# Kernel optimization log

Measured on AMD Instinct MI355X. Metric: run time of the kernel, lower is better.

The kernel has to match this reference:

```python
import jax, jax.numpy as jnp
import numpy as np

N, FIN, H, O, K = 300000, 128, 64, 32, 5


def setup_inputs() -> dict:
    key = jax.random.key(0)
    ks = jax.random.split(key, 8)
    xav_uh = (2.0 / (FIN + H)) ** 0.5  # xavier_normal scale for Linear(FIN, H)
    xav_ho = (2.0 / (H + O)) ** 0.5
    return {
        "user": jax.random.normal(ks[0], (N, FIN), dtype=jnp.float32),
        "item": jax.random.normal(ks[1], (N, FIN), dtype=jnp.float32),
        "r": jax.random.randint(ks[2], (N,), 0, K),
        "c": jax.random.uniform(ks[3], (N,), dtype=jnp.float32),
        # relation-stacked Linear weights, torch layout [out, in] -> [K, H, FIN]
        "Wu": jax.random.normal(ks[4], (K, H, FIN), dtype=jnp.float32) * xav_uh,
        "bu": jnp.zeros((K, H), dtype=jnp.float32),
        "Wv": jax.random.normal(ks[5], (K, H, FIN), dtype=jnp.float32) * xav_uh,
        "bv": jnp.zeros((K, H), dtype=jnp.float32),
        "Wl": jax.random.normal(ks[6], (O, H), dtype=jnp.float32) * xav_ho,
        "bl": jnp.zeros((O,), dtype=jnp.float32),
    }


def reference(user, item, r, c, Wu, bu, Wv, bv, Wl, bl):
    # Per-row relation-indexed linear: out[i] = x[i] @ W[r[i]].T + b[r[i]]
    def rel_linear(x, W, b):
        allp = jnp.einsum("ni,khi->nkh", x, W) + b[None]  # [N, K, H]
        return jnp.take_along_axis(allp, r[:, None, None], axis=1)[:, 0, :]  # [N, H]

    u_next = c[:, None] * rel_linear(item, Wu, bu)  # messages from items to users
    v_next = c[:, None] * rel_linear(user, Wv, bv)  # messages from users to items
    u_out = jax.nn.relu(jax.nn.relu(u_next) @ Wl.T + bl)
    v_out = jax.nn.relu(jax.nn.relu(v_next) @ Wl.T + bl)
    return (u_out, v_out)
```

## Files before the change

### kernel.cpp

```cpp
#include <hip/hip_runtime.h>
#include <hip/hip_bf16.h>

#define N_ROWS 300000
#define FIN    128
#define HDIM   64
#define ODIM   32
#define KREL   5
#define BRT    128
#define NTT    ((N_ROWS + BRT - 1) / BRT)
#define TPB    4
#define NCHUNK ((NTT + TPB - 1) / TPB)

typedef __attribute__((ext_vector_type(8))) short bf8_t;
typedef __attribute__((ext_vector_type(4))) float f32x4;
typedef __attribute__((ext_vector_type(4))) unsigned int u32x4;

static __device__ __forceinline__ unsigned pk2(float lo, float hi) {
  __hip_bfloat162 h = __float22bfloat162_rn(make_float2(lo, hi));
  return *reinterpret_cast<unsigned*>(&h);
}

static __device__ __forceinline__ bf8_t cvt8(float4 a, float4 b) {
  u32x4 u;
  u.x = pk2(a.x, a.y);
  u.y = pk2(a.z, a.w);
  u.z = pk2(b.x, b.y);
  u.w = pk2(b.z, b.w);
  return __builtin_bit_cast(bf8_t, u);
}

static __device__ __forceinline__ void stbf4_pk(void* base, int byte, float4 v) {
  unsigned long long p = (unsigned long long)pk2(v.x, v.y)
                       | ((unsigned long long)pk2(v.z, v.w) << 32);
  *(unsigned long long*)((char*)base + byte) = p;
}

static __device__ __forceinline__ bf8_t lds_load16(const void* base, int byte) {
  return *(const bf8_t*)((const char*)base + byte);
}


__global__ __launch_bounds__(512, 1) void gcn_main(
    const float* __restrict__ user, const float* __restrict__ item,
    const int* __restrict__ r, const float* __restrict__ c,
    const float* __restrict__ Wu, const float* __restrict__ bu,
    const float* __restrict__ Wv, const float* __restrict__ bv,
    const float* __restrict__ Wl, const float* __restrict__ bl,
    float* __restrict__ out)
{
  __shared__ __align__(16) unsigned short sW[KREL * HDIM * FIN];
  __shared__ __align__(16) unsigned short sX[BRT * FIN];
  __shared__ float sB[KREL * HDIM];

  const int tid   = threadIdx.x;
  const int side  = blockIdx.x & 1;
  const int chunk = blockIdx.x >> 1;
  const int t_begin = chunk * TPB;
  if (t_begin >= NTT) return;
  const int t_end = (t_begin + TPB < NTT) ? t_begin + TPB : NTT;

  const float* X  = side ? user : item;
  const float* Wk = side ? Wv : Wu;
  const float* bk = side ? bv : bu;

  const int lane = tid & 63;
  const int wid  = tid >> 6;
  const int lrow = lane & 15;
  const int lkg  = lane >> 4;
  const int sh   = lane >> 5;
  const int c4   = lane & 31;

  {
    const float4* w4 = (const float4*)Wk;
    #pragma unroll
    for (int j = 0; j < 20; ++j) {
      int f4   = j * 512 + tid;
      int k    = f4 >> 11;
      int rowk = (f4 >> 5) & 63;
      int cc   = f4 & 31;
      int byte = (k << 14) + ((rowk * 256 + cc * 8) ^ ((rowk & 7) << 4));
      stbf4_pk(sW, byte, w4[f4]);
    }
  }
  if (tid < KREL * HDIM) sB[tid] = bk[tid];

  bf8_t wl[2][2];
  #pragma unroll
  for (int n2 = 0; n2 < 2; ++n2)
    #pragma unroll
    for (int k2 = 0; k2 < 2; ++k2) {
      const float* p = Wl + (size_t)(n2 * 16 + lrow) * HDIM + k2 * 32 + lkg * 8;
      wl[n2][k2] = cvt8(*(const float4*)p, *(const float4*)(p + 4));
    }
  const float blv0 = bl[lrow];
  const float blv1 = bl[16 + lrow];

  char* myX = (char*)sX + wid * 4096;
  const int rowb_off = wid * 16;

  #pragma unroll
  for (int it = 0; it < 8; ++it) {
    int grow = t_begin * BRT + rowb_off + it * 2 + sh;
    grow = (grow < N_ROWS) ? grow : N_ROWS - 1;
    float4 a = *(const float4*)(X + (size_t)grow * FIN + c4 * 4);
    int rl   = it * 2 + sh;
    int byte = (rl * 256 + c4 * 8) ^ ((rl & 7) << 4);
    stbf4_pk(myX, byte, a);
  }
  __syncthreads();

  for (int t = t_begin; t < t_end; ++t) {
    const int tile0 = t * BRT;
    const bool do_stage = (t + 1 < t_end);

    int rowA = tile0 + rowb_off + lrow;
    int myrel = r[(rowA < N_ROWS) ? rowA : N_ROWS - 1];

    float4 ld[8];
    if (do_stage) {
      #pragma unroll
      for (int it = 0; it < 8; ++it) {
        int grow = tile0 + BRT + rowb_off + it * 2 + sh;
        grow = (grow < N_ROWS) ? grow : N_ROWS - 1;
        ld[it] = *(const float4*)(X + (size_t)grow * FIN + c4 * 4);
      }
    }

    const int erow = tile0 + rowb_off + lkg * 4;
    int rQ[4]; float cQ[4];
    #pragma unroll
    for (int q = 0; q < 4; ++q) {
      int rc = erow + q;
      rc = (rc < N_ROWS) ? rc : N_ROWS - 1;
      rQ[q] = r[rc];
      cQ[q] = c[rc];
    }

    __builtin_amdgcn_sched_barrier(0);

    f32x4 acc[4];
    #pragma unroll
    for (int n = 0; n < 4; ++n) acc[n] = f32x4{0.f, 0.f, 0.f, 0.f};

    const bf8_t zero8 = {};
    const int axor = (lrow & 7) << 4;
    #pragma unroll
    for (int kc = 0; kc < 4; ++kc) {
      const int kb = (kc * 32 + lkg * 8) * 2;
      bf8_t au = lds_load16(myX, (lrow * 256 + kb) ^ axor);
      #pragma unroll
      for (int k = 0; k < KREL; ++k) {
        bf8_t auk = (myrel == k) ? au : zero8;
        const int kofs = k << 14;
        #pragma unroll
        for (int n = 0; n < 4; ++n) {
          int brow = n * 16 + lrow;
          int bx   = kofs + ((brow * 256 + kb) ^ ((brow & 7) << 4));
          acc[n] = __builtin_amdgcn_mfma_f32_16x16x32_bf16(auk, lds_load16(sW, bx), acc[n], 0, 0, 0);
        }
      }
    }

    #pragma unroll
    for (int n = 0; n < 4; ++n) {
      int hcol = n * 16 + lrow;
      #pragma unroll
      for (int q = 0; q < 4; ++q) {
        int rr   = lkg * 4 + q;
        int byte = (rr * 128 + hcol * 2) ^ ((rr & 7) << 4);
        float bb = sB[rQ[q] * HDIM + hcol];
        float hv = fmaxf(cQ[q] * (acc[n][q] + bb), 0.f);
        *(unsigned short*)(myX + byte) = (unsigned short)(pk2(hv, hv) & 0xFFFFu);
      }
    }

    f32x4 acc2[2];
    acc2[0] = f32x4{0.f, 0.f, 0.f, 0.f};
    acc2[1] = f32x4{0.f, 0.f, 0.f, 0.f};
    #pragma unroll
    for (int k2 = 0; k2 < 2; ++k2) {
      const int kb = (k2 * 32 + lkg * 8) * 2;
      const int ax = (lrow * 128 + kb) ^ axor;
      bf8_t a2 = lds_load16(myX, ax);
      #pragma unroll
      for (int n2 = 0; n2 < 2; ++n2)
        acc2[n2] = __builtin_amdgcn_mfma_f32_16x16x32_bf16(a2, wl[n2][k2], acc2[n2], 0, 0, 0);
    }

    const size_t obase = (size_t)side * N_ROWS * ODIM;
    #pragma unroll
    for (int n2 = 0; n2 < 2; ++n2) {
      int col  = n2 * 16 + lrow;
      float bb = (n2 == 0) ? blv0 : blv1;
      #pragma unroll
      for (int q = 0; q < 4; ++q) {
        int row = erow + q;
        if (row < N_ROWS)
          out[obase + (size_t)row * ODIM + col] = fmaxf(acc2[n2][q] + bb, 0.f);
      }
    }

    __builtin_amdgcn_sched_barrier(0);

    if (do_stage) {
      #pragma unroll
      for (int it = 0; it < 8; ++it) {
        int rl   = it * 2 + sh;
        int byte = (rl * 256 + c4 * 8) ^ ((rl & 7) << 4);
        stbf4_pk(myX, byte, ld[it]);
      }
    }
  }
}

extern "C" void kernel_launch(void* const* d_in, const int* in_sizes, int n_in,
                              void* d_out, int out_size, void* d_ws, size_t ws_size,
                              hipStream_t stream) {
  const float* user = (const float*)d_in[0];
  const float* item = (const float*)d_in[1];
  const int*   r    = (const int*)d_in[2];
  const float* c    = (const float*)d_in[3];
  const float* Wu   = (const float*)d_in[4];
  const float* bu   = (const float*)d_in[5];
  const float* Wv   = (const float*)d_in[6];
  const float* bv   = (const float*)d_in[7];
  const float* Wl   = (const float*)d_in[8];
  const float* bl   = (const float*)d_in[9];
  float* out = (float*)d_out;

  gcn_main<<<2 * NCHUNK, 512, 0, stream>>>(user, item, r, c, Wu, bu, Wv, bv,
                                           Wl, bl, out);
}
```

Before: 113.3 us.

## Process two 16-row M-tiles per wave to reuse LDS weight fragments

Each wave now handles 32 rows instead of 16: the block tile grows to 256 rows and tiles per block drop to 2. Every weight fragment read from LDS feeds two MFMAs, halving weight LDS traffic per row, and the prefetch depth per thread doubles to 16 float4s. The cost is higher register pressure (twice the accumulators and staged loads) and an sX buffer that doubles to 64KB, bringing total LDS to about 146KB.

New measurement: 134.6 us. 18.8% more time.

```diff
diff --git a/kernel.cpp b/kernel.cpp
--- a/kernel.cpp
+++ b/kernel.cpp
@@ -6,9 +6,9 @@
 #define HDIM   64
 #define ODIM   32
 #define KREL   5
-#define BRT    128
+#define BRT    256
 #define NTT    ((N_ROWS + BRT - 1) / BRT)
-#define TPB    4
+#define TPB    2
 #define NCHUNK ((NTT + TPB - 1) / TPB)
 
 typedef __attribute__((ext_vector_type(8))) short bf8_t;
@@ -95,11 +95,11 @@
   const float blv0 = bl[lrow];
   const float blv1 = bl[16 + lrow];
 
-  char* myX = (char*)sX + wid * 4096;
-  const int rowb_off = wid * 16;
+  char* myX = (char*)sX + wid * 8192;
+  const int rowb_off = wid * 32;
 
   #pragma unroll
-  for (int it = 0; it < 8; ++it) {
+  for (int it = 0; it < 16; ++it) {
     int grow = t_begin * BRT + rowb_off + it * 2 + sh;
     grow = (grow < N_ROWS) ? grow : N_ROWS - 1;
     float4 a = *(const float4*)(X + (size_t)grow * FIN + c4 * 4);
@@ -112,51 +112,63 @@
   for (int t = t_begin; t < t_end; ++t) {
     const int tile0 = t * BRT;
     const bool do_stage = (t + 1 < t_end);
-
-    int rowA = tile0 + rowb_off + lrow;
-    int myrel = r[(rowA < N_ROWS) ? rowA : N_ROWS - 1];
-
-    float4 ld[8];
+    const int base = tile0 + rowb_off;
+
+    int ra0 = base + lrow;        ra0 = (ra0 < N_ROWS) ? ra0 : N_ROWS - 1;
+    int ra1 = base + 16 + lrow;   ra1 = (ra1 < N_ROWS) ? ra1 : N_ROWS - 1;
+    const int myrel0 = r[ra0];
+    const int myrel1 = r[ra1];
+
+    float4 ld[16];
     if (do_stage) {
       #pragma unroll
-      for (int it = 0; it < 8; ++it) {
-        int grow = tile0 + BRT + rowb_off + it * 2 + sh;
+      for (int it = 0; it < 16; ++it) {
+        int grow = base + BRT + it * 2 + sh;
         grow = (grow < N_ROWS) ? grow : N_ROWS - 1;
         ld[it] = *(const float4*)(X + (size_t)grow * FIN + c4 * 4);
       }
     }
 
-    const int erow = tile0 + rowb_off + lkg * 4;
-    int rQ[4]; float cQ[4];
-    #pragma unroll
-    for (int q = 0; q < 4; ++q) {
-      int rc = erow + q;
-      rc = (rc < N_ROWS) ? rc : N_ROWS - 1;
-      rQ[q] = r[rc];
-      cQ[q] = c[rc];
+    int rQ[2][4]; float cQ[2][4];
+    #pragma unroll
+    for (int h = 0; h < 2; ++h) {
+      #pragma unroll
+      for (int q = 0; q < 4; ++q) {
+        int rc = base + h * 16 + lkg * 4 + q;
+        rc = (rc < N_ROWS) ? rc : N_ROWS - 1;
+        rQ[h][q] = r[rc];
+        cQ[h][q] = c[rc];
+      }
     }
 
     __builtin_amdgcn_sched_barrier(0);
 
-    f32x4 acc[4];
-    #pragma unroll
-    for (int n = 0; n < 4; ++n) acc[n] = f32x4{0.f, 0.f, 0.f, 0.f};
+    f32x4 acc0[4], acc1[4];
+    #pragma unroll
+    for (int n = 0; n < 4; ++n) {
+      acc0[n] = f32x4{0.f, 0.f, 0.f, 0.f};
+      acc1[n] = f32x4{0.f, 0.f, 0.f, 0.f};
+    }
 
     const bf8_t zero8 = {};
     const int axor = (lrow & 7) << 4;
     #pragma unroll
     for (int kc = 0; kc < 4; ++kc) {
       const int kb = (kc * 32 + lkg * 8) * 2;
-      bf8_t au = lds_load16(myX, (lrow * 256 + kb) ^ axor);
+      bf8_t au0 = lds_load16(myX, ((lrow)      * 256 + kb) ^ axor);
+      bf8_t au1 = lds_load16(myX, ((16 + lrow) * 256 + kb) ^ axor);
       #pragma unroll
       for (int k = 0; k < KREL; ++k) {
-        bf8_t auk = (myrel == k) ? au : zero8;
+        bf8_t a0 = (myrel0 == k) ? au0 : zero8;
+        bf8_t a1 = (myrel1 == k) ? au1 : zero8;
         const int kofs = k << 14;
         #pragma unroll
         for (int n = 0; n < 4; ++n) {
           int brow = n * 16 + lrow;
           int bx   = kofs + ((brow * 256 + kb) ^ ((brow & 7) << 4));
-          acc[n] = __builtin_amdgcn_mfma_f32_16x16x32_bf16(auk, lds_load16(sW, bx), acc[n], 0, 0, 0);
+          bf8_t w = lds_load16(sW, bx);
+          acc0[n] = __builtin_amdgcn_mfma_f32_16x16x32_bf16(a0, w, acc0[n], 0, 0, 0);
+          acc1[n] = __builtin_amdgcn_mfma_f32_16x16x32_bf16(a1, w, acc1[n], 0, 0, 0);
         }
       }
     }
@@ -166,25 +178,39 @@
       int hcol = n * 16 + lrow;
       #pragma unroll
       for (int q = 0; q < 4; ++q) {
-        int rr   = lkg * 4 + q;
-        int byte = (rr * 128 + hcol * 2) ^ ((rr & 7) << 4);
-        float bb = sB[rQ[q] * HDIM + hcol];
-        float hv = fmaxf(cQ[q] * (acc[n][q] + bb), 0.f);
-        *(unsigned short*)(myX + byte) = (unsigned short)(pk2(hv, hv) & 0xFFFFu);
-      }
-    }
-
-    f32x4 acc2[2];
-    acc2[0] = f32x4{0.f, 0.f, 0.f, 0.f};
-    acc2[1] = f32x4{0.f, 0.f, 0.f, 0.f};
+        {
+          int rr   = lkg * 4 + q;
+          int byte = (rr * 128 + hcol * 2) ^ ((rr & 7) << 4);
+          float bb = sB[rQ[0][q] * HDIM + hcol];
+          float hv = fmaxf(cQ[0][q] * (acc0[n][q] + bb), 0.f);
+          *(unsigned short*)(myX + byte) = (unsigned short)(pk2(hv, hv) & 0xFFFFu);
+        }
+        {
+          int rr   = 16 + lkg * 4 + q;
+          int byte = (rr * 128 + hcol * 2) ^ ((rr & 7) << 4);
+          float bb = sB[rQ[1][q] * HDIM + hcol];
+          float hv = fmaxf(cQ[1][q] * (acc1[n][q] + bb), 0.f);
+          *(unsigned short*)(myX + byte) = (unsigned short)(pk2(hv, hv) & 0xFFFFu);
+        }
+      }
+    }
+
+    f32x4 acc2_0[2], acc2_1[2];
+    #pragma unroll
+    for (int n2 = 0; n2 < 2; ++n2) {
+      acc2_0[n2] = f32x4{0.f, 0.f, 0.f, 0.f};
+      acc2_1[n2] = f32x4{0.f, 0.f, 0.f, 0.f};
+    }
     #pragma unroll
     for (int k2 = 0; k2 < 2; ++k2) {
       const int kb = (k2 * 32 + lkg * 8) * 2;
-      const int ax = (lrow * 128 + kb) ^ axor;
-      bf8_t a2 = lds_load16(myX, ax);
-      #pragma unroll
-      for (int n2 = 0; n2 < 2; ++n2)
-        acc2[n2] = __builtin_amdgcn_mfma_f32_16x16x32_bf16(a2, wl[n2][k2], acc2[n2], 0, 0, 0);
+      bf8_t a20 = lds_load16(myX, ((lrow)      * 128 + kb) ^ axor);
+      bf8_t a21 = lds_load16(myX, ((16 + lrow) * 128 + kb) ^ axor);
+      #pragma unroll
+      for (int n2 = 0; n2 < 2; ++n2) {
+        acc2_0[n2] = __builtin_amdgcn_mfma_f32_16x16x32_bf16(a20, wl[n2][k2], acc2_0[n2], 0, 0, 0);
+        acc2_1[n2] = __builtin_amdgcn_mfma_f32_16x16x32_bf16(a21, wl[n2][k2], acc2_1[n2], 0, 0, 0);
+      }
     }
 
     const size_t obase = (size_t)side * N_ROWS * ODIM;
@@ -194,9 +220,12 @@
       float bb = (n2 == 0) ? blv0 : blv1;
       #pragma unroll
       for (int q = 0; q < 4; ++q) {
-        int row = erow + q;
-        if (row < N_ROWS)
-          out[obase + (size_t)row * ODIM + col] = fmaxf(acc2[n2][q] + bb, 0.f);
+        int row0 = base + lkg * 4 + q;
+        int row1 = base + 16 + lkg * 4 + q;
+        if (row0 < N_ROWS)
+          out[obase + (size_t)row0 * ODIM + col] = fmaxf(acc2_0[n2][q] + bb, 0.f);
+        if (row1 < N_ROWS)
+          out[obase + (size_t)row1 * ODIM + col] = fmaxf(acc2_1[n2][q] + bb, 0.f);
       }
     }
 
@@ -204,7 +233,7 @@
 
     if (do_stage) {
       #pragma unroll
-      for (int it = 0; it < 8; ++it) {
+      for (int it = 0; it < 16; ++it) {
         int rl   = it * 2 + sh;
         int byte = (rl * 256 + c4 * 8) ^ ((rl & 7) << 4);
         stbf4_pk(myX, byte, ld[it]);
```

## Sort tile rows by relation and skip absent relations per wavefront

Applied to the files above, without the earlier changes.

Each block counting-sorts the rows of its tiles by relation index in shared memory, then gathers input rows in that sorted order so each 16-row wavefront slice holds mostly one relation. The MFMA loop is restructured to run over relations outermost and skip any relation no lane in the wavefront needs, cutting the five-fold masked matmul work. This adds a shared-memory atomic sort, extra barriers, gathered (less coalesced) input loads and scattered output stores.

Measured after the change: 99.48 us (median of 2 runs). -12.2%, faster.

```diff
diff --git a/kernel.cpp b/kernel.cpp
--- a/kernel.cpp
+++ b/kernel.cpp
@@ -51,6 +51,9 @@
   __shared__ __align__(16) unsigned short sW[KREL * HDIM * FIN];
   __shared__ __align__(16) unsigned short sX[BRT * FIN];
   __shared__ float sB[KREL * HDIM];
+  __shared__ int sSrc[TPB][BRT];
+  __shared__ int sRel[TPB][BRT];
+  __shared__ int sCnt[TPB][KREL];
 
   const int tid   = threadIdx.x;
   const int side  = blockIdx.x & 1;
@@ -69,6 +72,27 @@
   const int lkg  = lane >> 4;
   const int sh   = lane >> 5;
   const int c4   = lane & 31;
+
+  {
+    const int j = tid >> 7;
+    const int i = tid & 127;
+    int tj = (t_begin + j < NTT) ? t_begin + j : NTT - 1;
+    int grow = tj * BRT + i;
+    int rr = r[(grow < N_ROWS) ? grow : N_ROWS - 1];
+    if (tid < TPB * KREL) sCnt[tid / KREL][tid % KREL] = 0;
+    __syncthreads();
+    int rank = atomicAdd(&sCnt[j][rr], 1);
+    __syncthreads();
+    if (tid < TPB) {
+      int off = 0;
+      #pragma unroll
+      for (int k = 0; k < KREL; ++k) { int v = sCnt[tid][k]; sCnt[tid][k] = off; off += v; }
+    }
+    __syncthreads();
+    int pos = sCnt[j][rr] + rank;
+    sSrc[j][pos] = i;
+    sRel[j][pos] = rr;
+  }
 
   {
     const float4* w4 = (const float4*)Wk;
@@ -98,42 +122,46 @@
   char* myX = (char*)sX + wid * 4096;
   const int rowb_off = wid * 16;
 
+  __syncthreads();
+
   #pragma unroll
   for (int it = 0; it < 8; ++it) {
-    int grow = t_begin * BRT + rowb_off + it * 2 + sh;
+    int slot = rowb_off + it * 2 + sh;
+    int grow = t_begin * BRT + sSrc[0][slot];
     grow = (grow < N_ROWS) ? grow : N_ROWS - 1;
     float4 a = *(const float4*)(X + (size_t)grow * FIN + c4 * 4);
     int rl   = it * 2 + sh;
     int byte = (rl * 256 + c4 * 8) ^ ((rl & 7) << 4);
     stbf4_pk(myX, byte, a);
   }
-  __syncthreads();
 
   for (int t = t_begin; t < t_end; ++t) {
+    const int j = t - t_begin;
     const int tile0 = t * BRT;
     const bool do_stage = (t + 1 < t_end);
 
-    int rowA = tile0 + rowb_off + lrow;
-    int myrel = r[(rowA < N_ROWS) ? rowA : N_ROWS - 1];
+    const int myrel = sRel[j][rowb_off + lrow];
 
     float4 ld[8];
     if (do_stage) {
       #pragma unroll
       for (int it = 0; it < 8; ++it) {
-        int grow = tile0 + BRT + rowb_off + it * 2 + sh;
+        int slot = rowb_off + it * 2 + sh;
+        int grow = (t + 1) * BRT + sSrc[j + 1][slot];
         grow = (grow < N_ROWS) ? grow : N_ROWS - 1;
         ld[it] = *(const float4*)(X + (size_t)grow * FIN + c4 * 4);
       }
     }
 
-    const int erow = tile0 + rowb_off + lkg * 4;
-    int rQ[4]; float cQ[4];
+    int lsrcQ[4], rQ[4]; float cQ[4];
     #pragma unroll
     for (int q = 0; q < 4; ++q) {
-      int rc = erow + q;
-      rc = (rc < N_ROWS) ? rc : N_ROWS - 1;
-      rQ[q] = r[rc];
-      cQ[q] = c[rc];
+      int slot = rowb_off + lkg * 4 + q;
+      int ls   = sSrc[j][slot];
+      lsrcQ[q] = ls;
+      rQ[q]    = sRel[j][slot];
+      int rc   = tile0 + ls;
+      cQ[q]    = c[(rc < N_ROWS) ? rc : N_ROWS - 1];
     }
 
     __builtin_amdgcn_sched_barrier(0);
@@ -144,19 +172,26 @@
 
     const bf8_t zero8 = {};
     const int axor = (lrow & 7) << 4;
+    bf8_t au[4];
     #pragma unroll
     for (int kc = 0; kc < 4; ++kc) {
       const int kb = (kc * 32 + lkg * 8) * 2;
-      bf8_t au = lds_load16(myX, (lrow * 256 + kb) ^ axor);
-      #pragma unroll
-      for (int k = 0; k < KREL; ++k) {
-        bf8_t auk = (myrel == k) ? au : zero8;
+      au[kc] = lds_load16(myX, (lrow * 256 + kb) ^ axor);
+    }
+    #pragma unroll
+    for (int k = 0; k < KREL; ++k) {
+      if (__any(myrel == k)) {
         const int kofs = k << 14;
         #pragma unroll
-        for (int n = 0; n < 4; ++n) {
-          int brow = n * 16 + lrow;
-          int bx   = kofs + ((brow * 256 + kb) ^ ((brow & 7) << 4));
-          acc[n] = __builtin_amdgcn_mfma_f32_16x16x32_bf16(auk, lds_load16(sW, bx), acc[n], 0, 0, 0);
+        for (int kc = 0; kc < 4; ++kc) {
+          const int kb = (kc * 32 + lkg * 8) * 2;
+          bf8_t auk = (myrel == k) ? au[kc] : zero8;
+          #pragma unroll
+          for (int n = 0; n < 4; ++n) {
+            int brow = n * 16 + lrow;
+            int bx   = kofs + ((brow * 256 + kb) ^ ((brow & 7) << 4));
+            acc[n] = __builtin_amdgcn_mfma_f32_16x16x32_bf16(auk, lds_load16(sW, bx), acc[n], 0, 0, 0);
+          }
         }
       }
     }
@@ -194,7 +229,7 @@
       float bb = (n2 == 0) ? blv0 : blv1;
       #pragma unroll
       for (int q = 0; q < 4; ++q) {
-        int row = erow + q;
+        int row = tile0 + lsrcQ[q];
         if (row < N_ROWS)
           out[obase + (size_t)row * ODIM + col] = fmaxf(acc2[n2][q] + bb, 0.f);
       }
```
